# Kernel tuning notes

Hardware: AMD Instinct MI355X
Metric: run time of the kernel (lower is better)

The kernel has to match this reference:

```python
import jax, jax.numpy as jnp
import numpy as np

EPS = 1e-5

def _bn2d(x, g, b, m, v):
    s = (1, -1, 1, 1)
    return (x - m.reshape(s)) * (g.reshape(s) * jax.lax.rsqrt(v.reshape(s) + EPS)) + b.reshape(s)

def _bn1d(x, g, b, m, v):
    return (x - m) * (g * jax.lax.rsqrt(v + EPS)) + b

def _conv3x3(x, w, b):
    y = jax.lax.conv_general_dilated(x, w, (1, 1), ((1, 1), (1, 1)),
                                     dimension_numbers=('NCHW', 'OIHW', 'NCHW'))
    return y + b.reshape(1, -1, 1, 1)

def setup_inputs() -> dict:
    key = jax.random.key(0)
    ks = iter(jax.random.split(key, 64))
    B = 512
    d = {}
    d['anchor'] = jax.random.normal(next(ks), (B, 1, 16, 8), jnp.float32)
    d['positive'] = jax.random.normal(next(ks), (B, 1, 16, 8), jnp.float32)
    d['negative'] = jax.random.normal(next(ks), (B, 1, 16, 8), jnp.float32)

    def bn_params(c):
        g = jax.random.normal(next(ks), (c,), jnp.float32) * 0.1 + 1.0
        b = jax.random.normal(next(ks), (c,), jnp.float32) * 0.1
        m = jax.random.normal(next(ks), (c,), jnp.float32) * 0.1
        v = jax.random.uniform(next(ks), (c,), jnp.float32, 0.5, 1.5)
        return g, b, m, v

    d['bn0_g'], d['bn0_b'], d['bn0_m'], d['bn0_v'] = bn_params(1)
    d['conv1_w'] = jax.random.normal(next(ks), (64, 1, 3, 3), jnp.float32) * 0.1
    d['conv1_b'] = jax.random.normal(next(ks), (64,), jnp.float32) * 0.1
    d['bn1_g'], d['bn1_b'], d['bn1_m'], d['bn1_v'] = bn_params(64)
    d['conv2_w'] = jax.random.normal(next(ks), (64, 64, 3, 3), jnp.float32) * 0.04
    d['conv2_b'] = jax.random.normal(next(ks), (64,), jnp.float32) * 0.1
    d['bn2_g'], d['bn2_b'], d['bn2_m'], d['bn2_v'] = bn_params(64)
    # locally-connected: kernel_size=1 -> per-position unshared channel mix (o,c,h,w)
    d['lc1_w'] = jax.random.normal(next(ks), (64, 64, 16, 8), jnp.float32) * 0.125
    d['bn3_g'], d['bn3_b'], d['bn3_m'], d['bn3_v'] = bn_params(64)
    d['lc2_w'] = jax.random.normal(next(ks), (64, 64, 16, 8), jnp.float32) * 0.125
    d['bn4_g'], d['bn4_b'], d['bn4_m'], d['bn4_v'] = bn_params(64)
    d['fc1_w'] = jax.random.normal(next(ks), (512, 8192), jnp.float32) * 0.01
    d['fc1_b'] = jax.random.normal(next(ks), (512,), jnp.float32) * 0.1
    d['bnf1_g'], d['bnf1_b'], d['bnf1_m'], d['bnf1_v'] = bn_params(512)
    d['fc2_w'] = jax.random.normal(next(ks), (512, 512), jnp.float32) * 0.04
    d['fc2_b'] = jax.random.normal(next(ks), (512,), jnp.float32) * 0.1
    d['bnf2_g'], d['bnf2_b'], d['bnf2_m'], d['bnf2_v'] = bn_params(512)
    d['fc3_w'] = jax.random.normal(next(ks), (128, 512), jnp.float32) * 0.04
    d['fc3_b'] = jax.random.normal(next(ks), (128,), jnp.float32) * 0.1
    d['bnf3_g'], d['bnf3_b'], d['bnf3_m'], d['bnf3_v'] = bn_params(128)
    d['out_w'] = jax.random.normal(next(ks), (128, 128), jnp.float32) * 0.09
    d['out_b'] = jax.random.normal(next(ks), (128,), jnp.float32) * 0.1
    return d

def _embedding(x, p):
    x = _bn2d(x, p['bn0_g'], p['bn0_b'], p['bn0_m'], p['bn0_v'])
    x = _conv3x3(x, p['conv1_w'], p['conv1_b'])
    x = jax.nn.relu(_bn2d(x, p['bn1_g'], p['bn1_b'], p['bn1_m'], p['bn1_v']))
    x = _conv3x3(x, p['conv2_w'], p['conv2_b'])
    x = jax.nn.relu(_bn2d(x, p['bn2_g'], p['bn2_b'], p['bn2_m'], p['bn2_v']))
    # locally connected (kernel 1): per-position channel mix, no huge unfold intermediate
    x = jnp.einsum('bchw,ochw->bohw', x, p['lc1_w'])
    x = jax.nn.relu(_bn2d(x, p['bn3_g'], p['bn3_b'], p['bn3_m'], p['bn3_v']))
    x = jnp.einsum('bchw,ochw->bohw', x, p['lc2_w'])
    x = jax.nn.relu(_bn2d(x, p['bn4_g'], p['bn4_b'], p['bn4_m'], p['bn4_v']))
    # dropout is identity in eval mode
    x = x.reshape(x.shape[0], -1)  # (B, 8192)
    x = x @ p['fc1_w'].T + p['fc1_b']
    x = jax.nn.relu(_bn1d(x, p['bnf1_g'], p['bnf1_b'], p['bnf1_m'], p['bnf1_v']))
    x = x @ p['fc2_w'].T + p['fc2_b']
    x = jax.nn.relu(_bn1d(x, p['bnf2_g'], p['bnf2_b'], p['bnf2_m'], p['bnf2_v']))
    x = x @ p['fc3_w'].T + p['fc3_b']
    x = jax.nn.relu(_bn1d(x, p['bnf3_g'], p['bnf3_b'], p['bnf3_m'], p['bnf3_v']))
    return x @ p['out_w'].T + p['out_b']

def reference(anchor, positive, negative,
              bn0_g, bn0_b, bn0_m, bn0_v,
              conv1_w, conv1_b, bn1_g, bn1_b, bn1_m, bn1_v,
              conv2_w, conv2_b, bn2_g, bn2_b, bn2_m, bn2_v,
              lc1_w, bn3_g, bn3_b, bn3_m, bn3_v,
              lc2_w, bn4_g, bn4_b, bn4_m, bn4_v,
              fc1_w, fc1_b, bnf1_g, bnf1_b, bnf1_m, bnf1_v,
              fc2_w, fc2_b, bnf2_g, bnf2_b, bnf2_m, bnf2_v,
              fc3_w, fc3_b, bnf3_g, bnf3_b, bnf3_m, bnf3_v,
              out_w, out_b):
    p = dict(bn0_g=bn0_g, bn0_b=bn0_b, bn0_m=bn0_m, bn0_v=bn0_v,
             conv1_w=conv1_w, conv1_b=conv1_b, bn1_g=bn1_g, bn1_b=bn1_b, bn1_m=bn1_m, bn1_v=bn1_v,
             conv2_w=conv2_w, conv2_b=conv2_b, bn2_g=bn2_g, bn2_b=bn2_b, bn2_m=bn2_m, bn2_v=bn2_v,
             lc1_w=lc1_w, bn3_g=bn3_g, bn3_b=bn3_b, bn3_m=bn3_m, bn3_v=bn3_v,
             lc2_w=lc2_w, bn4_g=bn4_g, bn4_b=bn4_b, bn4_m=bn4_m, bn4_v=bn4_v,
             fc1_w=fc1_w, fc1_b=fc1_b, bnf1_g=bnf1_g, bnf1_b=bnf1_b, bnf1_m=bnf1_m, bnf1_v=bnf1_v,
             fc2_w=fc2_w, fc2_b=fc2_b, bnf2_g=bnf2_g, bnf2_b=bnf2_b, bnf2_m=bnf2_m, bnf2_v=bnf2_v,
             fc3_w=fc3_w, fc3_b=fc3_b, bnf3_g=bnf3_g, bnf3_b=bnf3_b, bnf3_m=bnf3_m, bnf3_v=bnf3_v,
             out_w=out_w, out_b=out_b)
    return (_embedding(anchor, p), _embedding(positive, p), _embedding(negative, p))
```

## Files before the change

kernel.cpp:

```cpp
#include <hip/hip_runtime.h>
#include <math.h>

#define EPS 1e-5f
#define FD 8192

typedef __attribute__((ext_vector_type(8))) __bf16 bf16x8;
typedef __attribute__((ext_vector_type(4))) float f32x4;

static __device__ __forceinline__ f32x4 mfma16(bf16x8 a, bf16x8 b, f32x4 c) {
    return __builtin_amdgcn_mfma_f32_16x16x32_bf16(a, b, c, 0, 0, 0);
}

__global__ __launch_bounds__(256) void k_prep_all(
    const float* __restrict__ w1, const float* __restrict__ w2,
    const float* __restrict__ lc1, const float* __restrict__ lc2,
    const float* __restrict__ fc1w, const float* __restrict__ fc2w,
    const float* __restrict__ fc3w, const float* __restrict__ outw,
    __bf16* __restrict__ w1frag, __bf16* __restrict__ w2frag,
    __bf16* __restrict__ lc1frag, __bf16* __restrict__ lc2frag,
    __bf16* __restrict__ fc1Wb, __bf16* __restrict__ wf23) {
    const int bb = blockIdx.x;
    const int t = threadIdx.x;
    __shared__ float wbuf[64][130];

// ... 13 lines not shown
        const int lane = id & 63;
        const int w = (id >> 6) & 3;
        const int chunk = (id >> 8) & 1;
        const int tap = id >> 9;
        const int q = lane >> 4, li = lane & 15;
        const int o = w * 16 + li;
        const int c0 = chunk * 32 + q * 8;
        bf16x8 v;
#pragma unroll
        for (int j = 0; j < 8; ++j)
            v[j] = (__bf16)w2[(o * 64 + c0 + j) * 9 + tap];
        *(bf16x8*)(w2frag + (size_t)id * 8) = v;
    } else if (bb < 147) {
        const int bx = bb - 19;
        const int layer = bx >> 6, o = bx & 63;
        const int wo = o >> 4, lo = o & 15;
        const float* src = (layer ? lc2 : lc1) + (size_t)o * 8192;
        __bf16* dst = layer ? lc2frag : lc1frag;
#pragma unroll
        for (int pass = 0; pass < 8; ++pass) {
            int i = pass * 1024 + t * 4;
            float4 v = *(const float4*)(src + i);
            int c = i >> 7, p = i & 127;
            wbuf[c][p + 0] = v.x; wbuf[c][p + 1] = v.y;
            wbuf[c][p + 2] = v.z; wbuf[c][p + 3] = v.w;
        }
        __syncthreads();
#pragma unroll
        for (int pass = 0; pass < 4; ++pass) {
            int slot = pass * 256 + t;
            int p = slot >> 3, chunk = (slot >> 2) & 1, q = slot & 3;
            bf16x8 v;
#pragma unroll
            for (int j = 0; j < 8; ++j)
                v[j] = (__bf16)wbuf[chunk * 32 + q * 8 + j][p];
            *(bf16x8*)(dst + ((size_t)((p * 2 + chunk) * 4 + wo) * 64 + q * 16 + lo) * 8) = v;
        }
    } else if (bb < 659) {
        const int n = bb - 147;
        const float* src = fc1w + (size_t)n * 8192;
        __bf16* dst = fc1Wb + (size_t)n * 8192;
#pragma unroll
        for (int pass = 0; pass < 8; ++pass) {
            int i = pass * 1024 + t * 4;
            float4 v = *(const float4*)(src + i);
            int c = i >> 7, p = i & 127;
            wbuf[c][p + 0] = v.x; wbuf[c][p + 1] = v.y;
            wbuf[c][p + 2] = v.z; wbuf[c][p + 3] = v.w;
        }
        __syncthreads();
#pragma unroll
        for (int pass = 0; pass < 16; ++pass) {
            int kA = (pass * 256 + t) * 2;
            int c = kA & 63, p = kA >> 6;
            __bf16 tmp[2];
            tmp[0] = (__bf16)wbuf[c][p];
            tmp[1] = (__bf16)wbuf[c + 1][p];
            *(unsigned int*)(dst + kA) = *(unsigned int*)tmp;
        }
    } else {
        int i = (bb - 659) * 256 + t;
        float v;
        if (i < 262144) v = fc2w[i];
        else if (i < 327680) v = fc3w[i - 262144];
        else v = outw[i - 327680];
        wf23[i] = (__bf16)v;
    }
}

__global__ __launch_bounds__(256) void k_conv_mfma(
    const float* __restrict__ inA, const float* __restrict__ inP, const float* __restrict__ inN,
    const float* __restrict__ bn0g, const float* __restrict__ bn0b,
    const float* __restrict__ bn0m, const float* __restrict__ bn0v,
    const __bf16* __restrict__ w1frag, const float* __restrict__ b1,
    const float* __restrict__ bn1g, const float* __restrict__ bn1b,
    const float* __restrict__ bn1m, const float* __restrict__ bn1v,
    const __bf16* __restrict__ w2frag, const float* __restrict__ b2,
    const float* __restrict__ bn2g, const float* __restrict__ bn2b,
    const float* __restrict__ bn2m, const float* __restrict__ bn2v,
    __bf16* __restrict__ act) {
    const int b = blockIdx.x, t = threadIdx.x;
    const int lane = t & 63, w = t >> 6;
    const int q = lane >> 4, li = lane & 15;
    const int n0 = w * 16;
    const float* src = (b < 512 ? inA : (b < 1024 ? inP : inN)) + (size_t)(b & 511) * 128;

    __shared__ __align__(16) float xpad[180];
    __shared__ __align__(16) __bf16 A1[128 * 40];
    __shared__ __align__(16) __bf16 Xp[18 * 12 * 72];
    __shared__ float s1[64], sh1[64], s2[64], sh2[64];

    bf16x8 w1f = *(const bf16x8*)(w1frag + (size_t)(w * 64 + lane) * 8);
    bf16x8 w2f[18];
#pragma unroll
    for (int tap = 0; tap < 9; ++tap)
#pragma unroll
        for (int ch = 0; ch < 2; ++ch)
            w2f[tap * 2 + ch] = *(const bf16x8*)(w2frag +
                ((size_t)((tap * 2 + ch) * 4 + w) * 64 + lane) * 8);

    {
        int* xz = (int*)Xp;
        for (int i = t; i < 7776; i += 256) xz[i] = 0;
        if (t < 180) xpad[t] = 0.f;
        if (t < 64) {
            float sa = bn1g[t] * rsqrtf(bn1v[t] + EPS);
            s1[t] = sa;
            sh1[t] = (b1[t] - bn1m[t]) * sa + bn1b[t];
            float sb = bn2g[t] * rsqrtf(bn2v[t] + EPS);
            s2[t] = sb;
            sh2[t] = (b2[t] - bn2m[t]) * sb + bn2b[t];
        }
    }
    __syncthreads();
    if (t < 128) {
        float s0 = bn0g[0] * rsqrtf(bn0v[0] + EPS);
        float v = (src[t] - bn0m[0]) * s0 + bn0b[0];
        xpad[((t >> 3) + 1) * 10 + (t & 7) + 1] = v;
    }
    __syncthreads();
    {
        int p = t >> 1, half = t & 1;
        int r = p >> 3, cl = p & 7;
        bf16x8 v0, v1;
#pragma unroll
        for (int jj = 0; jj < 8; ++jj) {
            int j = half * 16 + jj;
            v0[jj] = (j < 9) ? (__bf16)xpad[(r + j / 3) * 10 + cl + (j % 3)] : (__bf16)0.f;
            int j2 = half * 16 + 8 + jj;
            v1[jj] = (j2 < 9) ? (__bf16)xpad[(r + j2 / 3) * 10 + cl + (j2 % 3)] : (__bf16)0.f;
        }
        *(bf16x8*)&A1[p * 40 + half * 16] = v0;
        *(bf16x8*)&A1[p * 40 + half * 16 + 8] = v1;
    }
    __syncthreads();
    {
        const float sco = s1[n0 + li], sho = sh1[n0 + li];
        const int o = n0 + li;
#pragma unroll
        for (int m = 0; m < 8; ++m) {
            bf16x8 a = *(const bf16x8*)&A1[(m * 16 + li) * 40 + q * 8];
            f32x4 z = {0.f, 0.f, 0.f, 0.f};
            f32x4 d = mfma16(a, w1f, z);
#pragma unroll
            for (int r = 0; r < 4; ++r) {
                int p = m * 16 + q * 4 + r;
                float v = fmaxf(d[r] * sco + sho, 0.f);
                Xp[(((p >> 3) + 1) * 12 + (p & 7) + 1) * 72 + o] = (__bf16)v;
            }
        }
    }
    __syncthreads();
    f32x4 accA[4], accB[4];
#pragma unroll
    for (int i = 0; i < 4; ++i) {
        accA[i] = (f32x4){0.f, 0.f, 0.f, 0.f};
        accB[i] = (f32x4){0.f, 0.f, 0.f, 0.f};
    }
    {
        const int cl = li & 7;
#pragma unroll
        for (int mp = 0; mp < 4; ++mp) {
            const int r0 = mp * 4 + (li >> 3);
            const int base0 = (r0 * 12 + cl) * 72 + q * 8;
            const int base1 = base0 + 1728;
#pragma unroll
            for (int tap = 0; tap < 9; ++tap) {
                const int tofs = ((tap / 3) * 12 + (tap % 3)) * 72;
#pragma unroll
                for (int ch = 0; ch < 2; ++ch) {
                    bf16x8 a0 = *(const bf16x8*)&Xp[base0 + tofs + ch * 32];
                    bf16x8 a1 = *(const bf16x8*)&Xp[base1 + tofs + ch * 32];
                    accA[mp] = mfma16(a0, w2f[tap * 2 + ch], accA[mp]);
                    accB[mp] = mfma16(a1, w2f[tap * 2 + ch], accB[mp]);
                }
            }
        }
    }
    __syncthreads();
    {
        const float sco = s2[n0 + li], sho = sh2[n0 + li];
        const int o = n0 + li;
#pragma unroll
        for (int mp = 0; mp < 4; ++mp) {
#pragma unroll
            for (int r = 0; r < 4; ++r) {
                int p0 = mp * 32 + q * 4 + r;
                Xp[p0 * 72 + o] = (__bf16)fmaxf(accA[mp][r] * sco + sho, 0.f);
                Xp[(p0 + 16) * 72 + o] = (__bf16)fmaxf(accB[mp][r] * sco + sho, 0.f);
            }
        }
    }
    __syncthreads();
    {
        int p = t >> 1, half = t & 1;
        const __bf16* rp = Xp + p * 72 + half * 32;
        __bf16* ob = act + (size_t)b * FD + p * 64 + half * 32;
        bf16x8 v0 = *(const bf16x8*)rp;
        bf16x8 v1 = *(const bf16x8*)(rp + 8);
        bf16x8 v2 = *(const bf16x8*)(rp + 16);
        bf16x8 v3 = *(const bf16x8*)(rp + 24);
        *(bf16x8*)ob = v0;
        *(bf16x8*)(ob + 8) = v1;
        *(bf16x8*)(ob + 16) = v2;
        *(bf16x8*)(ob + 24) = v3;
    }
}

__global__ __launch_bounds__(256) void k_lc_mfma(
    const __bf16* __restrict__ lc1frag, const __bf16* __restrict__ lc2frag,
    const float* __restrict__ bn3g, const float* __restrict__ bn3b,
    const float* __restrict__ bn3m, const float* __restrict__ bn3v,
    const float* __restrict__ bn4g, const float* __restrict__ bn4b,
    const float* __restrict__ bn4m, const float* __restrict__ bn4v,
    __bf16* __restrict__ act) {
    const int p = blockIdx.x;
    const int b0 = blockIdx.y * 64;
    const int t = threadIdx.x;
    const int lane = t & 63, w = t >> 6;
    const int q = lane >> 4, li = lane & 15;
    const int n0 = w * 16;

    __shared__ __align__(16) __bf16 xs[64 * 72];
    __shared__ __align__(16) __bf16 ys[64 * 72];
    __shared__ float s3[64], sh3[64], s4[64], sh4[64];

    if (t < 64) {
        float sa = bn3g[t] * rsqrtf(bn3v[t] + EPS);
        s3[t] = sa; sh3[t] = bn3b[t] - bn3m[t] * sa;
        float sb = bn4g[t] * rsqrtf(bn4v[t] + EPS);
        s4[t] = sb; sh4[t] = bn4b[t] - bn4m[t] * sb;
    }
    {
        int s = t >> 2, cg = t & 3;
        const __bf16* rp = act + (size_t)(b0 + s) * FD + p * 64 + cg * 16;
        *(bf16x8*)&xs[s * 72 + cg * 16] = *(const bf16x8*)rp;
        *(bf16x8*)&xs[s * 72 + cg * 16 + 8] = *(const bf16x8*)(rp + 8);
    }
    bf16x8 w1a = *(const bf16x8*)(lc1frag + ((size_t)((p * 2 + 0) * 4 + w) * 64 + lane) * 8);
    bf16x8 w1b = *(const bf16x8*)(lc1frag + ((size_t)((p * 2 + 1) * 4 + w) * 64 + lane) * 8);
    bf16x8 w2a = *(const bf16x8*)(lc2frag + ((size_t)((p * 2 + 0) * 4 + w) * 64 + lane) * 8);
    bf16x8 w2b = *(const bf16x8*)(lc2frag + ((size_t)((p * 2 + 1) * 4 + w) * 64 + lane) * 8);
    __syncthreads();
    {
        const float sco = s3[n0 + li], sho = sh3[n0 + li];
#pragma unroll
        for (int m = 0; m < 4; ++m) {
            bf16x8 a0 = *(const bf16x8*)&xs[(m * 16 + li) * 72 + q * 8];
            bf16x8 a1 = *(const bf16x8*)&xs[(m * 16 + li) * 72 + 32 + q * 8];
            f32x4 acc = {0.f, 0.f, 0.f, 0.f};
            acc = mfma16(a0, w1a, acc);
            acc = mfma16(a1, w1b, acc);
#pragma unroll
            for (int r = 0; r < 4; ++r) {
                int bl = m * 16 + q * 4 + r;
                ys[bl * 72 + n0 + li] = (__bf16)fmaxf(acc[r] * sco + sho, 0.f);
            }
        }
    }
    __syncthreads();
    {
        const float sco = s4[n0 + li], sho = sh4[n0 + li];
#pragma unroll
        for (int m = 0; m < 4; ++m) {
            bf16x8 a0 = *(const bf16x8*)&ys[(m * 16 + li) * 72 + q * 8];
            bf16x8 a1 = *(const bf16x8*)&ys[(m * 16 + li) * 72 + 32 + q * 8];
            f32x4 acc = {0.f, 0.f, 0.f, 0.f};
            acc = mfma16(a0, w2a, acc);
            acc = mfma16(a1, w2b, acc);
#pragma unroll
            for (int r = 0; r < 4; ++r) {
                int bl = m * 16 + q * 4 + r;
                xs[bl * 72 + n0 + li] = (__bf16)fmaxf(acc[r] * sco + sho, 0.f);
            }
        }
    }
    __syncthreads();
    {
        int s = t >> 2, cg = t & 3;
        const __bf16* rp = xs + s * 72 + cg * 16;
        __bf16* ob = act + (size_t)(b0 + s) * FD + p * 64 + cg * 16;
        bf16x8 v0 = *(const bf16x8*)rp;
        bf16x8 v1 = *(const bf16x8*)(rp + 8);
        *(bf16x8*)ob = v0;
        *(bf16x8*)(ob + 8) = v1;
    }
}

__global__ __launch_bounds__(256) void k_fc1_mfma(
    const __bf16* __restrict__ A, const __bf16* __restrict__ Wb,
    float* __restrict__ part) {
    const int t = threadIdx.x;
    const int lane = t & 63, w = t >> 6;
    const int q = lane >> 4, li = lane & 15;
    const int m0 = blockIdx.x * 64, n0 = blockIdx.y * 128;
    const int k0 = blockIdx.z * 1024;
    const int wm = (w & 1) * 32, wn = (w >> 1) * 64;

    __shared__ __align__(16) __bf16 As[64 * 40];
    __shared__ __align__(16) __bf16 Bs[128 * 40];

    f32x4 acc[2][4];
#pragma unroll
    for (int i = 0; i < 2; ++i)
#pragma unroll
        for (int j = 0; j < 4; ++j) acc[i][j] = (f32x4){0.f, 0.f, 0.f, 0.f};

    const int rowA = (t & 127) >> 1, rowB = t >> 1, half = t & 1;
    const __bf16* Ag = A + (size_t)(m0 + rowA) * 8192 + k0 + half * 16;
    const __bf16* Bg = Wb + (size_t)(n0 + rowB) * 8192 + k0 + half * 16;

    bf16x8 pa0, pa1, pb0, pb1;
    pb0 = *(const bf16x8*)Bg;
    pb1 = *(const bf16x8*)(Bg + 8);
    if (t < 128) {
        pa0 = *(const bf16x8*)Ag;
        pa1 = *(const bf16x8*)(Ag + 8);
    }

    for (int step = 0; step < 32; ++step) {
        if (t < 128) {
            *(bf16x8*)&As[rowA * 40 + half * 16] = pa0;
            *(bf16x8*)&As[rowA * 40 + half * 16 + 8] = pa1;
        }
        *(bf16x8*)&Bs[rowB * 40 + half * 16] = pb0;
        *(bf16x8*)&Bs[rowB * 40 + half * 16 + 8] = pb1;
        __syncthreads();
        Ag += 32; Bg += 32;
        if (step < 31) {
            pb0 = *(const bf16x8*)Bg;
            pb1 = *(const bf16x8*)(Bg + 8);
            if (t < 128) {
                pa0 = *(const bf16x8*)Ag;
                pa1 = *(const bf16x8*)(Ag + 8);
            }
        }
        bf16x8 af[2], bfr[4];
#pragma unroll
        for (int i = 0; i < 2; ++i)
            af[i] = *(const bf16x8*)&As[(wm + i * 16 + li) * 40 + q * 8];
#pragma unroll
        for (int j = 0; j < 4; ++j)
            bfr[j] = *(const bf16x8*)&Bs[(wn + j * 16 + li) * 40 + q * 8];
#pragma unroll
        for (int i = 0; i < 2; ++i)
#pragma unroll
            for (int j = 0; j < 4; ++j)
                acc[i][j] = mfma16(af[i], bfr[j], acc[i][j]);
        __syncthreads();
    }
    float* pp = part + (size_t)blockIdx.z * 786432;
#pragma unroll
    for (int i = 0; i < 2; ++i) {
#pragma unroll
        for (int r = 0; r < 4; ++r) {
            int m = m0 + wm + i * 16 + q * 4 + r;
#pragma unroll
            for (int j = 0; j < 4; ++j) {
                int n = n0 + wn + j * 16 + li;
                pp[(size_t)m * 512 + n] = acc[i][j][r];
            }
        }
    }
}

__global__ void k_fc1_reduce(const float* __restrict__ part, const float* __restrict__ bias,
                             const float* __restrict__ g, const float* __restrict__ bb,
                             const float* __restrict__ mm, const float* __restrict__ vv,
                             __bf16* __restrict__ out) {
    int gi = blockIdx.x * 256 + threadIdx.x;
    size_t off = (size_t)gi * 4;
    float4 s = make_float4(0.f, 0.f, 0.f, 0.f);
#pragma unroll
    for (int z = 0; z < 8; ++z) {
        float4 v = *(const float4*)(part + (size_t)z * 786432 + off);
        s.x += v.x; s.y += v.y; s.z += v.z; s.w += v.w;
    }
    int n = (gi & 127) * 4;
    float r[4] = {s.x, s.y, s.z, s.w};
    __bf16 o4[4];
#pragma unroll
    for (int j = 0; j < 4; ++j) {
        float sc = g[n + j] * rsqrtf(vv[n + j] + EPS);
        float x = (r[j] + bias[n + j] - mm[n + j]) * sc + bb[n + j];
        o4[j] = (__bf16)fmaxf(x, 0.f);
    }
    *(uint2*)(out + off) = *(uint2*)o4;
}

__global__ __launch_bounds__(256) void k_fc2_mfma(
    const __bf16* __restrict__ A, const __bf16* __restrict__ W,
    const float* __restrict__ bias,
    const float* __restrict__ bng, const float* __restrict__ bnb,
    const float* __restrict__ bnm, const float* __restrict__ bnv,
    __bf16* __restrict__ out) {
    const int t = threadIdx.x;
    const int lane = t & 63, w = t >> 6;
    const int q = lane >> 4, li = lane & 15;
    const int m0 = blockIdx.x * 64, n0 = blockIdx.y * 64;
    const int wm = (w & 1) * 32, wn = (w >> 1) * 32;
    const int K = 512, N = 512;

    __shared__ __align__(16) __bf16 As[64 * 40];
    __shared__ __align__(16) __bf16 Bs[64 * 40];

    f32x4 acc[2][2];
#pragma unroll
    for (int i = 0; i < 2; ++i)
#pragma unroll
        for (int j = 0; j < 2; ++j) acc[i][j] = (f32x4){0.f, 0.f, 0.f, 0.f};

    const int row = (t & 127) >> 1, half = t & 1;
    const __bf16* g = (t < 128 ? A + (size_t)(m0 + row) * K
                               : W + (size_t)(n0 + row) * K) + half * 16;
    __bf16* ld = (t < 128 ? As : Bs) + row * 40 + half * 16;

    bf16x8 p0 = *(const bf16x8*)g;
    bf16x8 p1 = *(const bf16x8*)(g + 8);
    for (int k0 = 0; k0 < K; k0 += 32) {
        *(bf16x8*)ld = p0;
        *(bf16x8*)(ld + 8) = p1;
        __syncthreads();
        g += 32;
        if (k0 + 32 < K) {
            p0 = *(const bf16x8*)g;
            p1 = *(const bf16x8*)(g + 8);
        }
        bf16x8 af[2], bfr[2];
#pragma unroll
        for (int i = 0; i < 2; ++i)
            af[i] = *(const bf16x8*)&As[(wm + i * 16 + li) * 40 + q * 8];
#pragma unroll
        for (int j = 0; j < 2; ++j)
            bfr[j] = *(const bf16x8*)&Bs[(wn + j * 16 + li) * 40 + q * 8];
#pragma unroll
        for (int i = 0; i < 2; ++i)
#pragma unroll
            for (int j = 0; j < 2; ++j)
                acc[i][j] = mfma16(af[i], bfr[j], acc[i][j]);
        __syncthreads();
    }
    float bi[2], sc[2], hh[2];
#pragma unroll
    for (int j = 0; j < 2; ++j) {
        int n = n0 + wn + j * 16 + li;
        bi[j] = bias[n];
        sc[j] = bng[n] * rsqrtf(bnv[n] + EPS);
        hh[j] = bnb[n] - bnm[n] * sc[j];
    }
#pragma unroll
    for (int i = 0; i < 2; ++i) {
#pragma unroll
        for (int r = 0; r < 4; ++r) {
            int m = m0 + wm + i * 16 + q * 4 + r;
#pragma unroll
            for (int j = 0; j < 2; ++j) {
                int n = n0 + wn + j * 16 + li;
                float x = (acc[i][j][r] + bi[j]) * sc[j] + hh[j];
                out[(size_t)m * N + n] = (__bf16)fmaxf(x, 0.f);
            }
        }
    }
}

__global__ __launch_bounds__(256) void k_fc3out(
    const __bf16* __restrict__ A, const __bf16* __restrict__ W3,
    const __bf16* __restrict__ Wo,
    const float* __restrict__ b3,
    const float* __restrict__ bng, const float* __restrict__ bnb,
    const float* __restrict__ bnm, const float* __restrict__ bnv,
    const float* __restrict__ bo, float* __restrict__ out) {
    const int t = threadIdx.x;
    const int lane = t & 63, w = t >> 6;
    const int q = lane >> 4, li = lane & 15;
    const int m0 = blockIdx.x * 64;
    const int wn = w * 32;

    __shared__ __align__(16) __bf16 As[64 * 40];
    __shared__ __align__(16) __bf16 Bs[128 * 40];
    __shared__ __align__(16) __bf16 ysb[64 * 136];

    const int rowA = (t & 127) >> 1, rowB = t >> 1, half = t & 1;
    const __bf16* Ag = A + (size_t)(m0 + rowA) * 512 + half * 16;
    const __bf16* Bg = W3 + (size_t)rowB * 512 + half * 16;

    f32x4 acc[4][2];
#pragma unroll
    for (int i = 0; i < 4; ++i)
#pragma unroll
        for (int j = 0; j < 2; ++j) acc[i][j] = (f32x4){0.f, 0.f, 0.f, 0.f};

    bf16x8 pa0, pa1, pb0, pb1;
    pb0 = *(const bf16x8*)Bg;
    pb1 = *(const bf16x8*)(Bg + 8);
    if (t < 128) {
        pa0 = *(const bf16x8*)Ag;
        pa1 = *(const bf16x8*)(Ag + 8);
    }
    for (int step = 0; step < 16; ++step) {
        if (t < 128) {
            *(bf16x8*)&As[rowA * 40 + half * 16] = pa0;
            *(bf16x8*)&As[rowA * 40 + half * 16 + 8] = pa1;
        }
        *(bf16x8*)&Bs[rowB * 40 + half * 16] = pb0;
        *(bf16x8*)&Bs[rowB * 40 + half * 16 + 8] = pb1;
        __syncthreads();
        Ag += 32; Bg += 32;
        if (step < 15) {
            pb0 = *(const bf16x8*)Bg;
            pb1 = *(const bf16x8*)(Bg + 8);
            if (t < 128) {
                pa0 = *(const bf16x8*)Ag;
                pa1 = *(const bf16x8*)(Ag + 8);
            }
        }
        bf16x8 af[4], bfr[2];
#pragma unroll
        for (int i = 0; i < 4; ++i)
            af[i] = *(const bf16x8*)&As[(i * 16 + li) * 40 + q * 8];
#pragma unroll
        for (int j = 0; j < 2; ++j)
            bfr[j] = *(const bf16x8*)&Bs[(wn + j * 16 + li) * 40 + q * 8];
#pragma unroll
        for (int i = 0; i < 4; ++i)
#pragma unroll
            for (int j = 0; j < 2; ++j)
                acc[i][j] = mfma16(af[i], bfr[j], acc[i][j]);
        __syncthreads();
    }
    {
#pragma unroll
        for (int j = 0; j < 2; ++j) {
            int n = wn + j * 16 + li;
            float sc = bng[n] * rsqrtf(bnv[n] + EPS);
            float hh = bnb[n] - bnm[n] * sc;
            float bi = b3[n];
#pragma unroll
            for (int i = 0; i < 4; ++i)
#pragma unroll
                for (int r = 0; r < 4; ++r) {
                    int ml = i * 16 + q * 4 + r;
                    float x = (acc[i][j][r] + bi) * sc + hh;
                    ysb[ml * 136 + n] = (__bf16)fmaxf(x, 0.f);
                }
        }
    }
    __syncthreads();
    f32x4 acc2[4][2];
#pragma unroll
    for (int i = 0; i < 4; ++i)
#pragma unroll
        for (int j = 0; j < 2; ++j) acc2[i][j] = (f32x4){0.f, 0.f, 0.f, 0.f};
    const __bf16* Bg2 = Wo + (size_t)rowB * 128 + half * 16;
#pragma unroll
    for (int step = 0; step < 4; ++step) {
        *(bf16x8*)&Bs[rowB * 40 + half * 16] = *(const bf16x8*)(Bg2 + step * 32);
        *(bf16x8*)&Bs[rowB * 40 + half * 16 + 8] = *(const bf16x8*)(Bg2 + step * 32 + 8);
        __syncthreads();
        bf16x8 af[4], bfr[2];
#pragma unroll
        for (int i = 0; i < 4; ++i)
            af[i] = *(const bf16x8*)&ysb[(i * 16 + li) * 136 + step * 32 + q * 8];
#pragma unroll
        for (int j = 0; j < 2; ++j)
            bfr[j] = *(const bf16x8*)&Bs[(wn + j * 16 + li) * 40 + q * 8];
#pragma unroll
        for (int i = 0; i < 4; ++i)
#pragma unroll
            for (int j = 0; j < 2; ++j)
                acc2[i][j] = mfma16(af[i], bfr[j], acc2[i][j]);
        __syncthreads();
    }
#pragma unroll
    for (int j = 0; j < 2; ++j) {
        int n = wn + j * 16 + li;
        float bi = bo[n];
#pragma unroll
        for (int i = 0; i < 4; ++i)
#pragma unroll
            for (int r = 0; r < 4; ++r) {
                int m = m0 + i * 16 + q * 4 + r;
                out[(size_t)m * 128 + n] = acc2[i][j][r] + bi;
            }
    }
}

extern "C" void kernel_launch(void* const* d_in, const int* in_sizes, int n_in,
                              void* d_out, int out_size, void* d_ws, size_t ws_size,
                              hipStream_t stream) {
    const float* inA    = (const float*)d_in[0];
    const float* inP    = (const float*)d_in[1];
    const float* inN    = (const float*)d_in[2];
    const float* bn0g   = (const float*)d_in[3];
    const float* bn0b   = (const float*)d_in[4];
    const float* bn0m   = (const float*)d_in[5];
    const float* bn0v   = (const float*)d_in[6];
    const float* conv1w = (const float*)d_in[7];
    const float* conv1b = (const float*)d_in[8];
    const float* bn1g   = (const float*)d_in[9];
    const float* bn1b   = (const float*)d_in[10];
    const float* bn1m   = (const float*)d_in[11];
    const float* bn1v   = (const float*)d_in[12];
    const float* conv2w = (const float*)d_in[13];
    const float* conv2b = (const float*)d_in[14];
    const float* bn2g   = (const float*)d_in[15];
    const float* bn2b   = (const float*)d_in[16];
    const float* bn2m   = (const float*)d_in[17];
    const float* bn2v   = (const float*)d_in[18];
    const float* lc1w   = (const float*)d_in[19];
    const float* bn3g   = (const float*)d_in[20];
    const float* bn3b   = (const float*)d_in[21];
    const float* bn3m   = (const float*)d_in[22];
    const float* bn3v   = (const float*)d_in[23];
    const float* lc2w   = (const float*)d_in[24];
    const float* bn4g   = (const float*)d_in[25];
    const float* bn4b   = (const float*)d_in[26];
    const float* bn4m   = (const float*)d_in[27];
    const float* bn4v   = (const float*)d_in[28];
    const float* fc1w   = (const float*)d_in[29];
    const float* fc1b   = (const float*)d_in[30];
    const float* bnf1g  = (const float*)d_in[31];
    const float* bnf1b  = (const float*)d_in[32];
    const float* bnf1m  = (const float*)d_in[33];
    const float* bnf1v  = (const float*)d_in[34];
    const float* fc2w   = (const float*)d_in[35];
    const float* fc2b   = (const float*)d_in[36];
    const float* bnf2g  = (const float*)d_in[37];
    const float* bnf2b  = (const float*)d_in[38];
    const float* bnf2m  = (const float*)d_in[39];
    const float* bnf2v  = (const float*)d_in[40];
    const float* fc3w   = (const float*)d_in[41];
    const float* fc3b   = (const float*)d_in[42];
    const float* bnf3g  = (const float*)d_in[43];
    const float* bnf3b  = (const float*)d_in[44];
    const float* bnf3m  = (const float*)d_in[45];
    const float* bnf3v  = (const float*)d_in[46];
    const float* outw   = (const float*)d_in[47];
    const float* outb   = (const float*)d_in[48];

    char* wsb = (char*)d_ws;
    __bf16* w1frag  = (__bf16*)wsb;
    __bf16* w2frag  = w1frag + 2048;
    __bf16* lc1frag = w2frag + 36864;
    __bf16* lc2frag = lc1frag + 524288;
    __bf16* fc1Wb   = lc2frag + 524288;
    __bf16* wf23    = fc1Wb + 4194304;
    __bf16* act     = wf23 + 344064;
    __bf16* act3    = act + 12582912;
    __bf16* act4    = act3 + 786432;
    float*  part    = (float*)(((uintptr_t)(act4 + 786432) + 15) & ~(uintptr_t)15);
    __bf16* wf2 = wf23;
    __bf16* wf3 = wf23 + 262144;
    __bf16* wfo = wf23 + 327680;

    k_prep_all<<<2003, 256, 0, stream>>>(conv1w, conv2w, lc1w, lc2w,
        fc1w, fc2w, fc3w, outw, w1frag, w2frag, lc1frag, lc2frag, fc1Wb, wf23);

    k_conv_mfma<<<1536, 256, 0, stream>>>(inA, inP, inN,
        bn0g, bn0b, bn0m, bn0v, w1frag, conv1b, bn1g, bn1b, bn1m, bn1v,
        w2frag, conv2b, bn2g, bn2b, bn2m, bn2v, act);

    k_lc_mfma<<<dim3(128, 24), 256, 0, stream>>>(lc1frag, lc2frag,
        bn3g, bn3b, bn3m, bn3v, bn4g, bn4b, bn4m, bn4v, act);

    k_fc1_mfma<<<dim3(24, 4, 8), 256, 0, stream>>>(act, fc1Wb, part);
    k_fc1_reduce<<<768, 256, 0, stream>>>(part, fc1b, bnf1g, bnf1b, bnf1m, bnf1v, act3);

    k_fc2_mfma<<<dim3(24, 8), 256, 0, stream>>>(act3, wf2, fc2b,
        bnf2g, bnf2b, bnf2m, bnf2v, act4);

    k_fc3out<<<24, 256, 0, stream>>>(act4, wf3, wfo, fc3b,
        bnf3g, bnf3b, bnf3m, bnf3v, outb, (float*)d_out);
}
```

Measured before the change: 249.0 us.

## Swap MFMA operand roles so outputs land channel-contiguous for packed LDS stores

In the conv and locally-connected kernels, the weight fragments become the A operand and activations the B operand of the MFMA. Each MFMA result row now holds 4 consecutive output channels, so results are written to shared memory as packed 8-byte stores instead of scattered 2-byte stores. Waves are re-tiled as 2 output-channel groups by 2 spatial or batch groups, each loading two weight fragments. This cuts LDS store instructions and bank conflicts in the epilogues and reuses each activation fragment across two MFMAs, at the cost of more weight registers per wave (36 bf16x8 for conv2).

```diff
diff --git a/kernel.cpp b/kernel.cpp
--- a/kernel.cpp
+++ b/kernel.cpp
@@ -119,7 +119,8 @@
     const int b = blockIdx.x, t = threadIdx.x;
     const int lane = t & 63, w = t >> 6;
     const int q = lane >> 4, li = lane & 15;
-    const int n0 = w * 16;
+    const int wo = w & 1;
+    const int wv = w >> 1;
     const float* src = (b < 512 ? inA : (b < 1024 ? inP : inN)) + (size_t)(b & 511) * 128;
 
     __shared__ __align__(16) float xpad[180];
@@ -127,14 +128,19 @@
     __shared__ __align__(16) __bf16 Xp[18 * 12 * 72];
     __shared__ float s1[64], sh1[64], s2[64], sh2[64];
 
-    bf16x8 w1f = *(const bf16x8*)(w1frag + (size_t)(w * 64 + lane) * 8);
-    bf16x8 w2f[18];
+    bf16x8 w1f[2];
+#pragma unroll
+    for (int mf = 0; mf < 2; ++mf)
+        w1f[mf] = *(const bf16x8*)(w1frag + (size_t)((wo * 2 + mf) * 64 + lane) * 8);
+    bf16x8 w2f[9][2][2];
 #pragma unroll
     for (int tap = 0; tap < 9; ++tap)
 #pragma unroll
         for (int ch = 0; ch < 2; ++ch)
-            w2f[tap * 2 + ch] = *(const bf16x8*)(w2frag +
-                ((size_t)((tap * 2 + ch) * 4 + w) * 64 + lane) * 8);
+#pragma unroll
+            for (int mf = 0; mf < 2; ++mf)
+                w2f[tap][ch][mf] = *(const bf16x8*)(w2frag +
+                    ((size_t)((tap * 2 + ch) * 4 + wo * 2 + mf) * 64 + lane) * 8);
 
     {
         int* xz = (int*)Xp;
@@ -172,61 +178,76 @@
     }
     __syncthreads();
     {
-        const float sco = s1[n0 + li], sho = sh1[n0 + li];
-        const int o = n0 + li;
-#pragma unroll
-        for (int m = 0; m < 8; ++m) {
-            bf16x8 a = *(const bf16x8*)&A1[(m * 16 + li) * 40 + q * 8];
-            f32x4 z = {0.f, 0.f, 0.f, 0.f};
-            f32x4 d = mfma16(a, w1f, z);
+        float sc[2][4], sh[2][4];
+#pragma unroll
+        for (int mf = 0; mf < 2; ++mf)
 #pragma unroll
             for (int r = 0; r < 4; ++r) {
-                int p = m * 16 + q * 4 + r;
-                float v = fmaxf(d[r] * sco + sho, 0.f);
-                Xp[(((p >> 3) + 1) * 12 + (p & 7) + 1) * 72 + o] = (__bf16)v;
-            }
-        }
-    }
-    __syncthreads();
-    f32x4 accA[4], accB[4];
-#pragma unroll
-    for (int i = 0; i < 4; ++i) {
-        accA[i] = (f32x4){0.f, 0.f, 0.f, 0.f};
-        accB[i] = (f32x4){0.f, 0.f, 0.f, 0.f};
-    }
-    {
-        const int cl = li & 7;
-#pragma unroll
-        for (int mp = 0; mp < 4; ++mp) {
-            const int r0 = mp * 4 + (li >> 3);
-            const int base0 = (r0 * 12 + cl) * 72 + q * 8;
-            const int base1 = base0 + 1728;
+                int o = wo * 32 + mf * 16 + q * 4 + r;
+                sc[mf][r] = s1[o]; sh[mf][r] = sh1[o];
+            }
+#pragma unroll
+        for (int nf = 0; nf < 4; ++nf) {
+            const int p = wv * 64 + nf * 16 + li;
+            bf16x8 bfr = *(const bf16x8*)&A1[p * 40 + q * 8];
+            const int pr = p >> 3, pc = p & 7;
+#pragma unroll
+            for (int mf = 0; mf < 2; ++mf) {
+                f32x4 z = {0.f, 0.f, 0.f, 0.f};
+                f32x4 d = mfma16(w1f[mf], bfr, z);
+                __bf16 o4[4];
+#pragma unroll
+                for (int r = 0; r < 4; ++r)
+                    o4[r] = (__bf16)fmaxf(d[r] * sc[mf][r] + sh[mf][r], 0.f);
+                *(uint2*)&Xp[((pr + 1) * 12 + pc + 1) * 72 + wo * 32 + mf * 16 + q * 4] =
+                    *(uint2*)o4;
+            }
+        }
+    }
+    __syncthreads();
+    f32x4 acc[2][4];
+#pragma unroll
+    for (int i = 0; i < 2; ++i)
+#pragma unroll
+        for (int j = 0; j < 4; ++j) acc[i][j] = (f32x4){0.f, 0.f, 0.f, 0.f};
+    {
+#pragma unroll
+        for (int nf = 0; nf < 4; ++nf) {
+            const int pr = wv * 8 + nf * 2 + (li >> 3), pc = li & 7;
+            const int base = (pr * 12 + pc) * 72 + q * 8;
 #pragma unroll
             for (int tap = 0; tap < 9; ++tap) {
                 const int tofs = ((tap / 3) * 12 + (tap % 3)) * 72;
 #pragma unroll
                 for (int ch = 0; ch < 2; ++ch) {
-                    bf16x8 a0 = *(const bf16x8*)&Xp[base0 + tofs + ch * 32];
-                    bf16x8 a1 = *(const bf16x8*)&Xp[base1 + tofs + ch * 32];
-                    accA[mp] = mfma16(a0, w2f[tap * 2 + ch], accA[mp]);
-                    accB[mp] = mfma16(a1, w2f[tap * 2 + ch], accB[mp]);
+                    bf16x8 bfr = *(const bf16x8*)&Xp[base + tofs + ch * 32];
+                    acc[0][nf] = mfma16(w2f[tap][ch][0], bfr, acc[0][nf]);
+                    acc[1][nf] = mfma16(w2f[tap][ch][1], bfr, acc[1][nf]);
                 }
             }
         }
     }
     __syncthreads();
     {
-        const float sco = s2[n0 + li], sho = sh2[n0 + li];
-        const int o = n0 + li;
-#pragma unroll
-        for (int mp = 0; mp < 4; ++mp) {
+        float sc[2][4], sh[2][4];
+#pragma unroll
+        for (int mf = 0; mf < 2; ++mf)
 #pragma unroll
             for (int r = 0; r < 4; ++r) {
-                int p0 = mp * 32 + q * 4 + r;
-                Xp[p0 * 72 + o] = (__bf16)fmaxf(accA[mp][r] * sco + sho, 0.f);
-                Xp[(p0 + 16) * 72 + o] = (__bf16)fmaxf(accB[mp][r] * sco + sho, 0.f);
-            }
-        }
+                int o = wo * 32 + mf * 16 + q * 4 + r;
+                sc[mf][r] = s2[o]; sh[mf][r] = sh2[o];
+            }
+#pragma unroll
+        for (int mf = 0; mf < 2; ++mf)
+#pragma unroll
+            for (int nf = 0; nf < 4; ++nf) {
+                __bf16 o4[4];
+#pragma unroll
+                for (int r = 0; r < 4; ++r)
+                    o4[r] = (__bf16)fmaxf(acc[mf][nf][r] * sc[mf][r] + sh[mf][r], 0.f);
+                int p = wv * 64 + nf * 16 + li;
+                *(uint2*)&Xp[p * 72 + wo * 32 + mf * 16 + q * 4] = *(uint2*)o4;
+            }
     }
     __syncthreads();
     {
@@ -256,7 +277,8 @@
     const int t = threadIdx.x;
     const int lane = t & 63, w = t >> 6;
     const int q = lane >> 4, li = lane & 15;
-    const int n0 = w * 16;
+    const int wo = w & 1;
+    const int wv = w >> 1;
 
     __shared__ __align__(16) __bf16 xs[64 * 72];
     __shared__ __align__(16) __bf16 ys[64 * 72];
@@ -274,41 +296,69 @@
         *(bf16x8*)&xs[s * 72 + cg * 16] = *(const bf16x8*)rp;
         *(bf16x8*)&xs[s * 72 + cg * 16 + 8] = *(const bf16x8*)(rp + 8);
     }
-    bf16x8 w1a = *(const bf16x8*)(lc1frag + ((size_t)((p * 2 + 0) * 4 + w) * 64 + lane) * 8);
-    bf16x8 w1b = *(const bf16x8*)(lc1frag + ((size_t)((p * 2 + 1) * 4 + w) * 64 + lane) * 8);
-    bf16x8 w2a = *(const bf16x8*)(lc2frag + ((size_t)((p * 2 + 0) * 4 + w) * 64 + lane) * 8);
-    bf16x8 w2b = *(const bf16x8*)(lc2frag + ((size_t)((p * 2 + 1) * 4 + w) * 64 + lane) * 8);
-    __syncthreads();
-    {
-        const float sco = s3[n0 + li], sho = sh3[n0 + li];
-#pragma unroll
-        for (int m = 0; m < 4; ++m) {
-            bf16x8 a0 = *(const bf16x8*)&xs[(m * 16 + li) * 72 + q * 8];
-            bf16x8 a1 = *(const bf16x8*)&xs[(m * 16 + li) * 72 + 32 + q * 8];
-            f32x4 acc = {0.f, 0.f, 0.f, 0.f};
-            acc = mfma16(a0, w1a, acc);
-            acc = mfma16(a1, w1b, acc);
+    bf16x8 wa[2][2], wb[2][2];
+#pragma unroll
+    for (int mf = 0; mf < 2; ++mf)
+#pragma unroll
+        for (int ks = 0; ks < 2; ++ks) {
+            wa[mf][ks] = *(const bf16x8*)(lc1frag +
+                ((size_t)((p * 2 + ks) * 4 + wo * 2 + mf) * 64 + lane) * 8);
+            wb[mf][ks] = *(const bf16x8*)(lc2frag +
+                ((size_t)((p * 2 + ks) * 4 + wo * 2 + mf) * 64 + lane) * 8);
+        }
+    __syncthreads();
+    {
+        float sc[2][4], sh[2][4];
+#pragma unroll
+        for (int mf = 0; mf < 2; ++mf)
 #pragma unroll
             for (int r = 0; r < 4; ++r) {
-                int bl = m * 16 + q * 4 + r;
-                ys[bl * 72 + n0 + li] = (__bf16)fmaxf(acc[r] * sco + sho, 0.f);
-            }
-        }
-    }
-    __syncthreads();
-    {
-        const float sco = s4[n0 + li], sho = sh4[n0 + li];
-#pragma unroll
-        for (int m = 0; m < 4; ++m) {
-            bf16x8 a0 = *(const bf16x8*)&ys[(m * 16 + li) * 72 + q * 8];
-            bf16x8 a1 = *(const bf16x8*)&ys[(m * 16 + li) * 72 + 32 + q * 8];
-            f32x4 acc = {0.f, 0.f, 0.f, 0.f};
-            acc = mfma16(a0, w2a, acc);
-            acc = mfma16(a1, w2b, acc);
+                int o = wo * 32 + mf * 16 + q * 4 + r;
+                sc[mf][r] = s3[o]; sh[mf][r] = sh3[o];
+            }
+#pragma unroll
+        for (int nf = 0; nf < 2; ++nf) {
+            int s = wv * 32 + nf * 16 + li;
+            bf16x8 x0 = *(const bf16x8*)&xs[s * 72 + q * 8];
+            bf16x8 x1 = *(const bf16x8*)&xs[s * 72 + 32 + q * 8];
+#pragma unroll
+            for (int mf = 0; mf < 2; ++mf) {
+                f32x4 acc = {0.f, 0.f, 0.f, 0.f};
+                acc = mfma16(wa[mf][0], x0, acc);
+                acc = mfma16(wa[mf][1], x1, acc);
+                __bf16 o4[4];
+#pragma unroll
+                for (int r = 0; r < 4; ++r)
+                    o4[r] = (__bf16)fmaxf(acc[r] * sc[mf][r] + sh[mf][r], 0.f);
+                *(uint2*)&ys[s * 72 + wo * 32 + mf * 16 + q * 4] = *(uint2*)o4;
+            }
+        }
+    }
+    __syncthreads();
+    {
+        float sc[2][4], sh[2][4];
+#pragma unroll
+        for (int mf = 0; mf < 2; ++mf)
 #pragma unroll
             for (int r = 0; r < 4; ++r) {
-                int bl = m * 16 + q * 4 + r;
-                xs[bl * 72 + n0 + li] = (__bf16)fmaxf(acc[r] * sco + sho, 0.f);
+                int o = wo * 32 + mf * 16 + q * 4 + r;
+                sc[mf][r] = s4[o]; sh[mf][r] = sh4[o];
+            }
+#pragma unroll
+        for (int nf = 0; nf < 2; ++nf) {
+            int s = wv * 32 + nf * 16 + li;
+            bf16x8 x0 = *(const bf16x8*)&ys[s * 72 + q * 8];
+            bf16x8 x1 = *(const bf16x8*)&ys[s * 72 + 32 + q * 8];
+#pragma unroll
+            for (int mf = 0; mf < 2; ++mf) {
+                f32x4 acc = {0.f, 0.f, 0.f, 0.f};
+                acc = mfma16(wb[mf][0], x0, acc);
+                acc = mfma16(wb[mf][1], x1, acc);
+                __bf16 o4[4];
+#pragma unroll
+                for (int r = 0; r < 4; ++r)
+                    o4[r] = (__bf16)fmaxf(acc[r] * sc[mf][r] + sh[mf][r], 0.f);
+                *(uint2*)&xs[s * 72 + wo * 32 + mf * 16 + q * 4] = *(uint2*)o4;
             }
         }
     }
```

New measurement: 260.2 us. +4.5%, slower.

## Fuse fc1 split-K reduce, fc2, fc3 and output layer into one kernel

Applied to the files above, without the earlier changes.

Replaces three kernels (fc1 partial reduction, fc2 GEMM, fc3+out GEMM) with one kernel that processes 32-row batch tiles. Each block reduces the fc1 partials into LDS, runs fc2 against the full weight with activations kept in LDS, then runs fc3 and the output layer. This removes two launches and the global round trips for the intermediate activations. In exchange only 48 blocks are launched, and each block streams the whole fc2 weight, so parallelism drops and redundant weight reads rise.

```diff
diff --git a/kernel.cpp b/kernel.cpp
--- a/kernel.cpp
+++ b/kernel.cpp
@@ -401,224 +401,200 @@
     }
 }
 
-__global__ void k_fc1_reduce(const float* __restrict__ part, const float* __restrict__ bias,
-                             const float* __restrict__ g, const float* __restrict__ bb,
-                             const float* __restrict__ mm, const float* __restrict__ vv,
-                             __bf16* __restrict__ out) {
-    int gi = blockIdx.x * 256 + threadIdx.x;
-    size_t off = (size_t)gi * 4;
-    float4 s = make_float4(0.f, 0.f, 0.f, 0.f);
-#pragma unroll
-    for (int z = 0; z < 8; ++z) {
-        float4 v = *(const float4*)(part + (size_t)z * 786432 + off);
-        s.x += v.x; s.y += v.y; s.z += v.z; s.w += v.w;
-    }
-    int n = (gi & 127) * 4;
-    float r[4] = {s.x, s.y, s.z, s.w};
-    __bf16 o4[4];
-#pragma unroll
-    for (int j = 0; j < 4; ++j) {
-        float sc = g[n + j] * rsqrtf(vv[n + j] + EPS);
-        float x = (r[j] + bias[n + j] - mm[n + j]) * sc + bb[n + j];
-        o4[j] = (__bf16)fmaxf(x, 0.f);
-    }
-    *(uint2*)(out + off) = *(uint2*)o4;
-}
-
-__global__ __launch_bounds__(256) void k_fc2_mfma(
-    const __bf16* __restrict__ A, const __bf16* __restrict__ W,
-    const float* __restrict__ bias,
-    const float* __restrict__ bng, const float* __restrict__ bnb,
-    const float* __restrict__ bnm, const float* __restrict__ bnv,
-    __bf16* __restrict__ out) {
+__global__ __launch_bounds__(256) void k_fc123out(
+    const float* __restrict__ part,
+    const float* __restrict__ b1, const float* __restrict__ g1,
+    const float* __restrict__ bb1, const float* __restrict__ m1,
+    const float* __restrict__ v1,
+    const __bf16* __restrict__ W2, const float* __restrict__ b2,
+    const float* __restrict__ g2, const float* __restrict__ bb2,
+    const float* __restrict__ m2, const float* __restrict__ v2,
+    const __bf16* __restrict__ W3, const float* __restrict__ b3,
+    const float* __restrict__ g3, const float* __restrict__ bb3,
+    const float* __restrict__ m3, const float* __restrict__ v3,
+    const __bf16* __restrict__ Wo, const float* __restrict__ bo,
+    float* __restrict__ out) {
     const int t = threadIdx.x;
     const int lane = t & 63, w = t >> 6;
     const int q = lane >> 4, li = lane & 15;
-    const int m0 = blockIdx.x * 64, n0 = blockIdx.y * 64;
-    const int wm = (w & 1) * 32, wn = (w >> 1) * 32;
-    const int K = 512, N = 512;
-
-    __shared__ __align__(16) __bf16 As[64 * 40];
-    __shared__ __align__(16) __bf16 Bs[64 * 40];
-
-    f32x4 acc[2][2];
-#pragma unroll
-    for (int i = 0; i < 2; ++i)
-#pragma unroll
-        for (int j = 0; j < 2; ++j) acc[i][j] = (f32x4){0.f, 0.f, 0.f, 0.f};
-
-    const int row = (t & 127) >> 1, half = t & 1;
-    const __bf16* g = (t < 128 ? A + (size_t)(m0 + row) * K
-                               : W + (size_t)(n0 + row) * K) + half * 16;
-    __bf16* ld = (t < 128 ? As : Bs) + row * 40 + half * 16;
-
-    bf16x8 p0 = *(const bf16x8*)g;
-    bf16x8 p1 = *(const bf16x8*)(g + 8);
-    for (int k0 = 0; k0 < K; k0 += 32) {
-        *(bf16x8*)ld = p0;
-        *(bf16x8*)(ld + 8) = p1;
-        __syncthreads();
-        g += 32;
-        if (k0 + 32 < K) {
-            p0 = *(const bf16x8*)g;
-            p1 = *(const bf16x8*)(g + 8);
-        }
-        bf16x8 af[2], bfr[2];
+    const int m0 = blockIdx.x * 32;
+    const int wn = w * 32;
+
+    __shared__ __align__(16) __bf16 As3[32 * 516];
+    __shared__ __align__(16) __bf16 A4[32 * 516];
+    __shared__ __align__(16) __bf16 Bs[128 * 40];
+    __shared__ __align__(16) __bf16 ysb[32 * 136];
+
+#pragma unroll
+    for (int i = 0; i < 16; ++i) {
+        int off = (i * 256 + t) * 4;
+        int row = off >> 9, col = off & 511;
+        size_t gofs = (size_t)(m0 + row) * 512 + col;
+        float4 s = make_float4(0.f, 0.f, 0.f, 0.f);
+#pragma unroll
+        for (int z = 0; z < 8; ++z) {
+            float4 v = *(const float4*)(part + (size_t)z * 786432 + gofs);
+            s.x += v.x; s.y += v.y; s.z += v.z; s.w += v.w;
+        }
+        float r4[4] = {s.x, s.y, s.z, s.w};
+        __bf16 o4[4];
+#pragma unroll
+        for (int j = 0; j < 4; ++j) {
+            int n = col + j;
+            float sc = g1[n] * rsqrtf(v1[n] + EPS);
+            float x = (r4[j] + b1[n] - m1[n]) * sc + bb1[n];
+            o4[j] = (__bf16)fmaxf(x, 0.f);
+        }
+        *(uint2*)&As3[row * 516 + col] = *(uint2*)o4;
+    }
+    __syncthreads();
+
+    const int rowB = t >> 1, half = t & 1;
+
+    {
+        f32x4 acc[2][2];
 #pragma unroll
         for (int i = 0; i < 2; ++i)
-            af[i] = *(const bf16x8*)&As[(wm + i * 16 + li) * 40 + q * 8];
-#pragma unroll
-        for (int j = 0; j < 2; ++j)
-            bfr[j] = *(const bf16x8*)&Bs[(wn + j * 16 + li) * 40 + q * 8];
+#pragma unroll
+            for (int j = 0; j < 2; ++j) acc[i][j] = (f32x4){0.f, 0.f, 0.f, 0.f};
+        const __bf16* Bg = W2 + (size_t)rowB * 512 + half * 16;
+        bf16x8 p0 = *(const bf16x8*)Bg;
+        bf16x8 p1 = *(const bf16x8*)(Bg + 8);
+        for (int s = 0; s < 64; ++s) {
+            *(bf16x8*)&Bs[rowB * 40 + half * 16] = p0;
+            *(bf16x8*)&Bs[rowB * 40 + half * 16 + 8] = p1;
+            __syncthreads();
+            if (s < 63) {
+                int s1 = s + 1;
+                const __bf16* Bg1 = W2 +
+                    ((size_t)((s1 >> 4) * 128 + rowB)) * 512 + (s1 & 15) * 32 + half * 16;
+                p0 = *(const bf16x8*)Bg1;
+                p1 = *(const bf16x8*)(Bg1 + 8);
+            }
+            const int ks = s & 15;
+            bf16x8 af[2], bfr[2];
+#pragma unroll
+            for (int i = 0; i < 2; ++i)
+                af[i] = *(const bf16x8*)&As3[(i * 16 + li) * 516 + ks * 32 + q * 8];
+#pragma unroll
+            for (int j = 0; j < 2; ++j)
+                bfr[j] = *(const bf16x8*)&Bs[(wn + j * 16 + li) * 40 + q * 8];
+#pragma unroll
+            for (int i = 0; i < 2; ++i)
+#pragma unroll
+                for (int j = 0; j < 2; ++j)
+                    acc[i][j] = mfma16(af[i], bfr[j], acc[i][j]);
+            __syncthreads();
+            if (ks == 15) {
+                const int nb = s >> 4;
+#pragma unroll
+                for (int j = 0; j < 2; ++j) {
+                    int n = nb * 128 + wn + j * 16 + li;
+                    float sc = g2[n] * rsqrtf(v2[n] + EPS);
+                    float hh = bb2[n] - m2[n] * sc;
+                    float bi = b2[n];
+#pragma unroll
+                    for (int i2 = 0; i2 < 2; ++i2) {
+#pragma unroll
+                        for (int r = 0; r < 4; ++r) {
+                            float x = (acc[i2][j][r] + bi) * sc + hh;
+                            A4[(i2 * 16 + q * 4 + r) * 516 + n] = (__bf16)fmaxf(x, 0.f);
+                        }
+                        acc[i2][j] = (f32x4){0.f, 0.f, 0.f, 0.f};
+                    }
+                }
+            }
+        }
+    }
+
+    {
+        f32x4 acc[2][2];
 #pragma unroll
         for (int i = 0; i < 2; ++i)
 #pragma unroll
+            for (int j = 0; j < 2; ++j) acc[i][j] = (f32x4){0.f, 0.f, 0.f, 0.f};
+        const __bf16* Bg = W3 + (size_t)rowB * 512 + half * 16;
+        bf16x8 p0 = *(const bf16x8*)Bg;
+        bf16x8 p1 = *(const bf16x8*)(Bg + 8);
+        for (int s = 0; s < 16; ++s) {
+            *(bf16x8*)&Bs[rowB * 40 + half * 16] = p0;
+            *(bf16x8*)&Bs[rowB * 40 + half * 16 + 8] = p1;
+            __syncthreads();
+            Bg += 32;
+            if (s < 15) {
+                p0 = *(const bf16x8*)Bg;
+                p1 = *(const bf16x8*)(Bg + 8);
+            }
+            bf16x8 af[2], bfr[2];
+#pragma unroll
+            for (int i = 0; i < 2; ++i)
+                af[i] = *(const bf16x8*)&A4[(i * 16 + li) * 516 + s * 32 + q * 8];
+#pragma unroll
             for (int j = 0; j < 2; ++j)
-                acc[i][j] = mfma16(af[i], bfr[j], acc[i][j]);
-        __syncthreads();
-    }
-    float bi[2], sc[2], hh[2];
-#pragma unroll
-    for (int j = 0; j < 2; ++j) {
-        int n = n0 + wn + j * 16 + li;
-        bi[j] = bias[n];
-        sc[j] = bng[n] * rsqrtf(bnv[n] + EPS);
-        hh[j] = bnb[n] - bnm[n] * sc[j];
-    }
-#pragma unroll
-    for (int i = 0; i < 2; ++i) {
-#pragma unroll
-        for (int r = 0; r < 4; ++r) {
-            int m = m0 + wm + i * 16 + q * 4 + r;
-#pragma unroll
-            for (int j = 0; j < 2; ++j) {
-                int n = n0 + wn + j * 16 + li;
-                float x = (acc[i][j][r] + bi[j]) * sc[j] + hh[j];
-                out[(size_t)m * N + n] = (__bf16)fmaxf(x, 0.f);
-            }
-        }
-    }
-}
-
-__global__ __launch_bounds__(256) void k_fc3out(
-    const __bf16* __restrict__ A, const __bf16* __restrict__ W3,
-    const __bf16* __restrict__ Wo,
-    const float* __restrict__ b3,
-    const float* __restrict__ bng, const float* __restrict__ bnb,
-    const float* __restrict__ bnm, const float* __restrict__ bnv,
-    const float* __restrict__ bo, float* __restrict__ out) {
-    const int t = threadIdx.x;
-    const int lane = t & 63, w = t >> 6;
-    const int q = lane >> 4, li = lane & 15;
-    const int m0 = blockIdx.x * 64;
-    const int wn = w * 32;
-
-    __shared__ __align__(16) __bf16 As[64 * 40];
-    __shared__ __align__(16) __bf16 Bs[128 * 40];
-    __shared__ __align__(16) __bf16 ysb[64 * 136];
-
-    const int rowA = (t & 127) >> 1, rowB = t >> 1, half = t & 1;
-    const __bf16* Ag = A + (size_t)(m0 + rowA) * 512 + half * 16;
-    const __bf16* Bg = W3 + (size_t)rowB * 512 + half * 16;
-
-    f32x4 acc[4][2];
-#pragma unroll
-    for (int i = 0; i < 4; ++i)
-#pragma unroll
-        for (int j = 0; j < 2; ++j) acc[i][j] = (f32x4){0.f, 0.f, 0.f, 0.f};
-
-    bf16x8 pa0, pa1, pb0, pb1;
-    pb0 = *(const bf16x8*)Bg;
-    pb1 = *(const bf16x8*)(Bg + 8);
-    if (t < 128) {
-        pa0 = *(const bf16x8*)Ag;
-        pa1 = *(const bf16x8*)(Ag + 8);
-    }
-    for (int step = 0; step < 16; ++step) {
-        if (t < 128) {
-            *(bf16x8*)&As[rowA * 40 + half * 16] = pa0;
-            *(bf16x8*)&As[rowA * 40 + half * 16 + 8] = pa1;
-        }
-        *(bf16x8*)&Bs[rowB * 40 + half * 16] = pb0;
-        *(bf16x8*)&Bs[rowB * 40 + half * 16 + 8] = pb1;
-        __syncthreads();
-        Ag += 32; Bg += 32;
-        if (step < 15) {
-            pb0 = *(const bf16x8*)Bg;
-            pb1 = *(const bf16x8*)(Bg + 8);
-            if (t < 128) {
-                pa0 = *(const bf16x8*)Ag;
-                pa1 = *(const bf16x8*)(Ag + 8);
-            }
-        }
-        bf16x8 af[4], bfr[2];
-#pragma unroll
-        for (int i = 0; i < 4; ++i)
-            af[i] = *(const bf16x8*)&As[(i * 16 + li) * 40 + q * 8];
-#pragma unroll
-        for (int j = 0; j < 2; ++j)
-            bfr[j] = *(const bf16x8*)&Bs[(wn + j * 16 + li) * 40 + q * 8];
-#pragma unroll
-        for (int i = 0; i < 4; ++i)
-#pragma unroll
-            for (int j = 0; j < 2; ++j)
-                acc[i][j] = mfma16(af[i], bfr[j], acc[i][j]);
-        __syncthreads();
-    }
-    {
+                bfr[j] = *(const bf16x8*)&Bs[(wn + j * 16 + li) * 40 + q * 8];
+#pragma unroll
+            for (int i = 0; i < 2; ++i)
+#pragma unroll
+                for (int j = 0; j < 2; ++j)
+                    acc[i][j] = mfma16(af[i], bfr[j], acc[i][j]);
+            __syncthreads();
+        }
 #pragma unroll
         for (int j = 0; j < 2; ++j) {
             int n = wn + j * 16 + li;
-            float sc = bng[n] * rsqrtf(bnv[n] + EPS);
-            float hh = bnb[n] - bnm[n] * sc;
+            float sc = g3[n] * rsqrtf(v3[n] + EPS);
+            float hh = bb3[n] - m3[n] * sc;
             float bi = b3[n];
 #pragma unroll
-            for (int i = 0; i < 4; ++i)
+            for (int i2 = 0; i2 < 2; ++i2)
 #pragma unroll
                 for (int r = 0; r < 4; ++r) {
-                    int ml = i * 16 + q * 4 + r;
-                    float x = (acc[i][j][r] + bi) * sc + hh;
+                    int ml = i2 * 16 + q * 4 + r;
+                    float x = (acc[i2][j][r] + bi) * sc + hh;
                     ysb[ml * 136 + n] = (__bf16)fmaxf(x, 0.f);
                 }
         }
     }
     __syncthreads();
-    f32x4 acc2[4][2];
-#pragma unroll
-    for (int i = 0; i < 4; ++i)
-#pragma unroll
-        for (int j = 0; j < 2; ++j) acc2[i][j] = (f32x4){0.f, 0.f, 0.f, 0.f};
-    const __bf16* Bg2 = Wo + (size_t)rowB * 128 + half * 16;
-#pragma unroll
-    for (int step = 0; step < 4; ++step) {
-        *(bf16x8*)&Bs[rowB * 40 + half * 16] = *(const bf16x8*)(Bg2 + step * 32);
-        *(bf16x8*)&Bs[rowB * 40 + half * 16 + 8] = *(const bf16x8*)(Bg2 + step * 32 + 8);
-        __syncthreads();
-        bf16x8 af[4], bfr[2];
-#pragma unroll
-        for (int i = 0; i < 4; ++i)
-            af[i] = *(const bf16x8*)&ysb[(i * 16 + li) * 136 + step * 32 + q * 8];
-#pragma unroll
-        for (int j = 0; j < 2; ++j)
-            bfr[j] = *(const bf16x8*)&Bs[(wn + j * 16 + li) * 40 + q * 8];
-#pragma unroll
-        for (int i = 0; i < 4; ++i)
+
+    {
+        f32x4 acc[2][2];
+#pragma unroll
+        for (int i = 0; i < 2; ++i)
+#pragma unroll
+            for (int j = 0; j < 2; ++j) acc[i][j] = (f32x4){0.f, 0.f, 0.f, 0.f};
+        const __bf16* Bg = Wo + (size_t)rowB * 128 + half * 16;
+#pragma unroll
+        for (int s = 0; s < 4; ++s) {
+            *(bf16x8*)&Bs[rowB * 40 + half * 16] = *(const bf16x8*)(Bg + s * 32);
+            *(bf16x8*)&Bs[rowB * 40 + half * 16 + 8] = *(const bf16x8*)(Bg + s * 32 + 8);
+            __syncthreads();
+            bf16x8 af[2], bfr[2];
+#pragma unroll
+            for (int i = 0; i < 2; ++i)
+                af[i] = *(const bf16x8*)&ysb[(i * 16 + li) * 136 + s * 32 + q * 8];
 #pragma unroll
             for (int j = 0; j < 2; ++j)
-                acc2[i][j] = mfma16(af[i], bfr[j], acc2[i][j]);
-        __syncthreads();
-    }
-#pragma unroll
-    for (int j = 0; j < 2; ++j) {
-        int n = wn + j * 16 + li;
-        float bi = bo[n];
-#pragma unroll
-        for (int i = 0; i < 4; ++i)
-#pragma unroll
-            for (int r = 0; r < 4; ++r) {
-                int m = m0 + i * 16 + q * 4 + r;
-                out[(size_t)m * 128 + n] = acc2[i][j][r] + bi;
-            }
+                bfr[j] = *(const bf16x8*)&Bs[(wn + j * 16 + li) * 40 + q * 8];
+#pragma unroll
+            for (int i = 0; i < 2; ++i)
+#pragma unroll
+                for (int j = 0; j < 2; ++j)
+                    acc[i][j] = mfma16(af[i], bfr[j], acc[i][j]);
+            __syncthreads();
+        }
+#pragma unroll
+        for (int j = 0; j < 2; ++j) {
+            int n = wn + j * 16 + li;
+            float bi = bo[n];
+#pragma unroll
+            for (int i2 = 0; i2 < 2; ++i2)
+#pragma unroll
+                for (int r = 0; r < 4; ++r) {
+                    int m = m0 + i2 * 16 + q * 4 + r;
+                    out[(size_t)m * 128 + n] = acc[i2][j][r] + bi;
+                }
+        }
     }
 }
 
@@ -701,11 +677,10 @@
         bn3g, bn3b, bn3m, bn3v, bn4g, bn4b, bn4m, bn4v, act);
 
     k_fc1_mfma<<<dim3(24, 4, 8), 256, 0, stream>>>(act, fc1Wb, part);
-    k_fc1_reduce<<<768, 256, 0, stream>>>(part, fc1b, bnf1g, bnf1b, bnf1m, bnf1v, act3);
-
-    k_fc2_mfma<<<dim3(24, 8), 256, 0, stream>>>(act3, wf2, fc2b,
-        bnf2g, bnf2b, bnf2m, bnf2v, act4);
-
-    k_fc3out<<<24, 256, 0, stream>>>(act4, wf3, wfo, fc3b,
-        bnf3g, bnf3b, bnf3m, bnf3v, outb, (float*)d_out);
+
+    k_fc123out<<<48, 256, 0, stream>>>(part,
+        fc1b, bnf1g, bnf1b, bnf1m, bnf1v,
+        wf2, fc2b, bnf2g, bnf2b, bnf2m, bnf2v,
+        wf3, fc3b, bnf3g, bnf3b, bnf3m, bnf3v,
+        wfo, outb, (float*)d_out);
 }
```

New measurement: 283.1 us. +13.7%, slower.
